# Optimization experiments

Measured on AMD Instinct MI355X. Metric: run time of the kernel, lower is better.

Reference implementation:

```python
import jax, jax.numpy as jnp
import numpy as np

D_MODEL = 1024
H = 16
D_K = D_MODEL // H

def setup_inputs() -> dict:
    key = jax.random.key(0)
    k1, k2, k3, k4, k5 = jax.random.split(key, 5)
    x = jax.random.normal(k1, (2, 2048, D_MODEL), dtype=jnp.float32)
    s = 1.0 / np.sqrt(D_MODEL)
    W_qkv = jax.random.uniform(k2, (D_MODEL, 3 * D_MODEL), jnp.float32, -s, s)
    b_qkv = jax.random.uniform(k3, (3 * D_MODEL,), jnp.float32, -s, s)
    W_o = jax.random.uniform(k4, (D_MODEL, D_MODEL), jnp.float32, -s, s)
    b_o = jax.random.uniform(k5, (D_MODEL,), jnp.float32, -s, s)
    return {"x": x, "W_qkv": W_qkv, "b_qkv": b_qkv, "W_o": W_o, "b_o": b_o}

def reference(x, W_qkv, b_qkv, W_o, b_o):
    B, L, _ = x.shape
    qkv = x @ W_qkv + b_qkv                      # [B, L, 3*d_model]
    q, k, v = jnp.split(qkv, 3, axis=-1)
    def split_heads(t):
        return t.reshape(B, L, H, D_K).transpose(0, 2, 1, 3)  # [B,H,L,D_k]
    q, k, v = split_heads(q), split_heads(k), split_heads(v)
    scores = jnp.einsum('bhqd,bhkd->bhqk', q, k) / np.sqrt(D_K).astype(jnp.float32)
    attn = jax.nn.softmax(scores, axis=-1)       # [B,H,L,L]
    ctx = jnp.einsum('bhqk,bhkd->bhqd', attn, v)
    ctx = ctx.transpose(0, 2, 1, 3).reshape(B, L, H * D_K)
    out = ctx @ W_o + b_o                        # dropout is identity at eval
    return (out, attn)
```

## Files before the change

kernel.cpp:

```cpp
#include <hip/hip_runtime.h>
#include <stdint.h>

typedef __attribute__((ext_vector_type(8))) short bf16x8;
typedef __attribute__((ext_vector_type(4))) float f32x4;
typedef __attribute__((ext_vector_type(4))) unsigned int u32x4;
typedef __attribute__((ext_vector_type(4))) unsigned short u16x4;

#define DEVINL static __device__ __forceinline__

DEVINL unsigned short f2bf(float f) {
  uint32_t u = __builtin_bit_cast(uint32_t, f);
  u = (u + 0x7FFFu + ((u >> 16) & 1u)) >> 16;
  return (unsigned short)u;
}

DEVINL float fexp2(float x) {
#if __has_builtin(__builtin_amdgcn_exp2f)
  return __builtin_amdgcn_exp2f(x);
#else
  return __expf(x * 0.69314718056f);
#endif
}

DEVINL bf16x8 pack8(f32x4 a, f32x4 b) {
  union { uint32_t u[4]; bf16x8 v; } r;
  asm("v_cvt_pk_bf16_f32 %0, %1, %2" : "=v"(r.u[0]) : "v"(a[0]), "v"(a[1]));
  asm("v_cvt_pk_bf16_f32 %0, %1, %2" : "=v"(r.u[1]) : "v"(a[2]), "v"(a[3]));
  asm("v_cvt_pk_bf16_f32 %0, %1, %2" : "=v"(r.u[2]) : "v"(b[0]), "v"(b[1]));
  asm("v_cvt_pk_bf16_f32 %0, %1, %2" : "=v"(r.u[3]) : "v"(b[2]), "v"(b[3]));
  return r.v;
}

DEVINL void async16(const unsigned short* lds, const unsigned short* g) {
  __builtin_amdgcn_global_load_lds(
      (const __attribute__((address_space(1))) unsigned int*)g,
      (__attribute__((address_space(3))) unsigned int*)lds, 16, 0, 0);
}

__global__ __launch_bounds__(256) void k_cast_x(const float* __restrict__ in,
                                                unsigned short* __restrict__ out, int n4) {
  int i = blockIdx.x * 256 + threadIdx.x;
  if (i >= n4) return;
  f32x4 v = *(const f32x4*)(in + (size_t)i * 4);
  u16x4 o;
  for (int j = 0; j < 4; ++j) o[j] = f2bf(v[j]);
  *(u16x4*)(out + (size_t)i * 4) = o;
}

__global__ __launch_bounds__(256) void k_transpose_w(const float* __restrict__ in,
                                                     unsigned short* __restrict__ out,
                                                     int K, int N) {
  __shared__ unsigned short tile[64][72];
  int k0 = blockIdx.x * 64, n0 = blockIdx.y * 64;
  int t = threadIdx.x;
  int r = t >> 2, c0 = (t & 3) * 16;
  for (int j = 0; j < 4; ++j) {
    int col = c0 + j * 4;
    f32x4 v = *(const f32x4*)(in + (size_t)(k0 + r) * N + n0 + col);
    u16x4 o;
    for (int q = 0; q < 4; ++q) o[q] = f2bf(v[q]);
    *(u16x4*)(&tile[r][col]) = o;
  }
  __syncthreads();
  for (int j = 0; j < 4; ++j) {
    int kcol = c0 + j * 4;
    u16x4 o;
    for (int q = 0; q < 4; ++q) o[q] = tile[kcol + q][r];
    *(u16x4*)(out + (size_t)(n0 + r) * K + k0 + kcol) = o;
  }
}

template <int MODE>
__global__ __launch_bounds__(256) void k_gemm(const unsigned short* __restrict__ A,
                                              const unsigned short* __restrict__ Bt,
                                              const float* __restrict__ bias,
                                              unsigned short* __restrict__ Qb,
                                              unsigned short* __restrict__ Kb,
                                              unsigned short* __restrict__ Vt,
                                              float* __restrict__ outF) {
  constexpr int KD = 1024;
  __shared__ unsigned short sh[17408];
  unsigned short* lA = sh;
  unsigned short* lB = sh + 8192;
  int tid = threadIdx.x;
  int lane = tid & 63, w = tid >> 6;
  int wr = w >> 1, wc = w & 1;
  int m0 = blockIdx.x * 128, n0 = blockIdx.y * 128;
  int lr = lane & 15, lg = lane >> 4;

  f32x4 acc[4][4] = {};

  int srow = w * 32 + (lane >> 3);
  int scol = (lane & 7) * 8;
  const unsigned short* gA = A + (size_t)(m0 + srow) * KD + scol;
  const unsigned short* gB = Bt + (size_t)(n0 + srow) * KD + scol;

  for (int kk = 0; kk < KD; kk += 64) {
    for (int s = 0; s < 4; ++s) {
      async16(&lA[(w * 32 + s * 8) * 64], gA + (size_t)s * 8 * KD + kk);
      async16(&lB[(w * 32 + s * 8) * 64], gB + (size_t)s * 8 * KD + kk);
    }
    __syncthreads();
    for (int kq = 0; kq < 2; ++kq) {
      bf16x8 af[4], bfr[4];
      for (int i = 0; i < 4; ++i)
        af[i] = *(const bf16x8*)(&lA[(wr * 64 + i * 16 + lr) * 64 + (kq * 4 + lg) * 8]);
      for (int r = 0; r < 4; ++r)
        bfr[r] = *(const bf16x8*)(&lB[(wc * 64 + r * 16 + lr) * 64 + (kq * 4 + lg) * 8]);
      for (int i = 0; i < 4; ++i)
        for (int r = 0; r < 4; ++r)
          acc[i][r] = __builtin_amdgcn_mfma_f32_16x16x32_bf16(af[i], bfr[r], acc[i][r], 0, 0, 0);
    }
    __syncthreads();
  }

  if (MODE == 0) {
    int which = n0 >> 10;
    int head0 = (n0 & 1023) >> 6;
    int b_idx = m0 >> 11;
    int l0 = m0 & 2047;
    if (which < 2) {
      for (int r = 0; r < 4; ++r) {
        int nl = wc * 64 + r * 16 + lr;
        float bv = bias[n0 + nl];
        for (int i = 0; i < 4; ++i) {
          int mlb = wr * 64 + i * 16 + lg * 4;
          for (int jj = 0; jj < 4; ++jj)
            sh[(mlb + jj) * 136 + nl] = f2bf(acc[i][r][jj] + bv);
        }
      }
      __syncthreads();
      unsigned short* dst = (which == 0) ? Qb : Kb;
      for (int it = 0; it < 4; ++it) {
        int row = it * 64 + (tid >> 2);
        int ml = row & 127, hd = row >> 7;
        int c = (tid & 3) * 16;
        bf16x8 v0 = *(const bf16x8*)&sh[ml * 136 + hd * 64 + c];
        bf16x8 v1 = *(const bf16x8*)&sh[ml * 136 + hd * 64 + c + 8];
        size_t bh = (size_t)(b_idx * 16 + head0 + hd);
        size_t off = (bh * 2048 + l0 + ml) * 64 + c;
        *(bf16x8*)(dst + off) = v0;
        *(bf16x8*)(dst + off + 8) = v1;
      }
    } else {
      for (int r = 0; r < 4; ++r) {
        int nl = wc * 64 + r * 16 + lr;
        float bv = bias[n0 + nl];
        for (int i = 0; i < 4; ++i) {
          int mlb = wr * 64 + i * 16 + lg * 4;
          u16x4 pk;
          for (int jj = 0; jj < 4; ++jj) pk[jj] = f2bf(acc[i][r][jj] + bv);
          *(u16x4*)&sh[nl * 136 + mlb] = pk;
        }
      }
      __syncthreads();
      for (int it = 0; it < 4; ++it) {
        int nl = it * 32 + (tid >> 3);
        int c = (tid & 7) * 16;
        bf16x8 v0 = *(const bf16x8*)&sh[nl * 136 + c];
        bf16x8 v1 = *(const bf16x8*)&sh[nl * 136 + c + 8];
        int dk = nl & 63, hd = nl >> 6;
        size_t bh = (size_t)(b_idx * 16 + head0 + hd);
        size_t off = (bh * 64 + dk) * 2048 + l0 + c;
        *(bf16x8*)(Vt + off) = v0;
        *(bf16x8*)(Vt + off + 8) = v1;
      }
    }
  } else {
    for (int r = 0; r < 4; ++r) {
      int n = n0 + wc * 64 + r * 16 + lr;
      float bv = bias[n];
      for (int i = 0; i < 4; ++i) {
        int mb = m0 + wr * 64 + i * 16 + lg * 4;
        for (int jj = 0; jj < 4; ++jj)
          outF[(size_t)(mb + jj) * 1024 + n] = acc[i][r][jj] + bv;
      }
    }
  }
}

__global__ __launch_bounds__(256) void k_attn(const unsigned short* __restrict__ Qb,
                                              const unsigned short* __restrict__ Kb,
                                              const unsigned short* __restrict__ Vt,
                                              float* __restrict__ attn,
                                              unsigned short* __restrict__ ctx) {
  __shared__ unsigned short Ks[64 * 64];
  __shared__ unsigned short Vs[64 * 64];
  __shared__ float Pf[4][32 * 68];
  int tid = threadIdx.x, lane = tid & 63, w = tid >> 6;
  int lr = lane & 15, lg = lane >> 4;
  int bid = blockIdx.x;
  int xcd = bid & 7, slot = bid >> 3;
  int bh = xcd * 4 + (slot >> 4);
  int qb = slot & 15;
  int q0 = qb * 128 + w * 32;
  int b_idx = bh >> 4, h = bh & 15;
  const unsigned short* Qh = Qb + (size_t)bh * 2048 * 64;
  const unsigned short* Kh = Kb + (size_t)bh * 2048 * 64;
  const unsigned short* Vh = Vt + (size_t)bh * 64 * 2048;
  float* Pw = &Pf[w][0];
  const float A2 = 0.125f * 1.44269504089f;
  int e7 = lr & 7;

  int srow = w * 8 + (lane >> 3);
  int sc = (lane & 7) ^ (srow & 7);
  const unsigned short* gK = Kh + (size_t)srow * 64 + sc * 8;
  const unsigned short* gV = Vh + (size_t)srow * 2048 + sc * 8;

  bf16x8 qf[2][2];
  for (int i = 0; i < 2; ++i)
    for (int kq = 0; kq < 2; ++kq)
      qf[i][kq] = *(const bf16x8*)(Qh + (size_t)(q0 + i * 16 + lr) * 64 + kq * 32 + lg * 8);

  float l_run[8] = {0.f, 0.f, 0.f, 0.f, 0.f, 0.f, 0.f, 0.f};

  for (int kt = 0; kt < 32; ++kt) {
    async16(&Ks[(w * 8) * 64],       gK + (size_t)kt * 4096);
    async16(&Ks[((w + 4) * 8) * 64], gK + (size_t)kt * 4096 + 2048);
    __syncthreads();
    f32x4 acc[2][4] = {};
    for (int kq = 0; kq < 2; ++kq) {
      int j = kq * 4 + lg;
      bf16x8 kf[4];
      for (int r = 0; r < 4; ++r)
        kf[r] = *(const bf16x8*)&Ks[(r * 16 + lr) * 64 + ((j ^ e7) << 3)];
      for (int i = 0; i < 2; ++i)
        for (int r = 0; r < 4; ++r)
          acc[i][r] = __builtin_amdgcn_mfma_f32_16x16x32_bf16(qf[i][kq], kf[r], acc[i][r], 0, 0, 0);
    }
    for (int i = 0; i < 2; ++i)
      for (int jj = 0; jj < 4; ++jj) {
        int z = i * 4 + jj;
        l_run[z] += fexp2(acc[i][0][jj] * A2) + fexp2(acc[i][1][jj] * A2) +
                    fexp2(acc[i][2][jj] * A2) + fexp2(acc[i][3][jj] * A2);
      }
    __syncthreads();
  }
  float invl[8];
  for (int z = 0; z < 8; ++z) {
    float s = l_run[z];
    s += __shfl_xor(s, 1);
    s += __shfl_xor(s, 2);
    s += __shfl_xor(s, 4);
    s += __shfl_xor(s, 8);
    invl[z] = 1.0f / s;
  }

  f32x4 cacc[2][4] = {};
  float* attn_base = attn + (size_t)bh * 2048 * 2048;
  float* arow = attn_base + (size_t)(q0 + lg) * 2048 + lr * 4;

  for (int kt = 0; kt < 32; ++kt) {
    async16(&Ks[(w * 8) * 64],       gK + (size_t)kt * 4096);
    async16(&Ks[((w + 4) * 8) * 64], gK + (size_t)kt * 4096 + 2048);
    async16(&Vs[(w * 8) * 64],       gV + (size_t)kt * 64);
    async16(&Vs[((w + 4) * 8) * 64], gV + (size_t)kt * 64 + 65536);
    __syncthreads();
    f32x4 acc[2][4] = {};
    for (int kq = 0; kq < 2; ++kq) {
      int j = kq * 4 + lg;
      bf16x8 kf[4];
      for (int r = 0; r < 4; ++r)
        kf[r] = *(const bf16x8*)&Ks[(r * 16 + lr) * 64 + ((j ^ e7) << 3)];
      for (int i = 0; i < 2; ++i)
        for (int r = 0; r < 4; ++r)
          acc[i][r] = __builtin_amdgcn_mfma_f32_16x16x32_bf16(qf[i][kq], kf[r], acc[i][r], 0, 0, 0);
    }
    for (int i = 0; i < 2; ++i)
      for (int r = 0; r < 4; ++r) {
        int key = r * 16 + lr;
        for (int jj = 0; jj < 4; ++jj) {
          int z = i * 4 + jj;
          int rl = i * 16 + lg * 4 + jj;
          Pw[rl * 68 + key] = fexp2(acc[i][r][jj] * A2) * invl[z];
        }
      }
    for (int s = 0; s < 8; ++s) {
      f32x4 v = *(const f32x4*)(&Pw[(s * 4 + lg) * 68 + lr * 4]);
      __builtin_nontemporal_store(v, (f32x4*)(arow + (size_t)s * 4 * 2048 + kt * 64));
    }
    for (int kq2 = 0; kq2 < 2; ++kq2) {
      int j = kq2 * 4 + lg;
      int kof = kq2 * 32 + lg * 8;
      bf16x8 pa[2], vf[4];
      for (int i = 0; i < 2; ++i) {
        f32x4 plo = *(const f32x4*)(&Pw[(i * 16 + lr) * 68 + kof]);
        f32x4 phi = *(const f32x4*)(&Pw[(i * 16 + lr) * 68 + kof + 4]);
        pa[i] = pack8(plo, phi);
      }
      for (int nn = 0; nn < 4; ++nn)
        vf[nn] = *(const bf16x8*)&Vs[(nn * 16 + lr) * 64 + ((j ^ e7) << 3)];
      for (int i = 0; i < 2; ++i)
        for (int nn = 0; nn < 4; ++nn)
          cacc[i][nn] = __builtin_amdgcn_mfma_f32_16x16x32_bf16(pa[i], vf[nn], cacc[i][nn], 0, 0, 0);
    }
    __syncthreads();
  }

  for (int nn = 0; nn < 4; ++nn) {
    int d = nn * 16 + lr;
    for (int i = 0; i < 2; ++i)
      for (int jj = 0; jj < 4; ++jj) {
        int q = q0 + i * 16 + lg * 4 + jj;
        int tok = b_idx * 2048 + q;
        ctx[(size_t)tok * 1024 + h * 64 + d] = f2bf(cacc[i][nn][jj]);
      }
  }
}

extern "C" void kernel_launch(void* const* d_in, const int* in_sizes, int n_in,
                              void* d_out, int out_size, void* d_ws, size_t ws_size,
                              hipStream_t stream) {
  const float* x    = (const float*)d_in[0];
  const float* Wqkv = (const float*)d_in[1];
  const float* bqkv = (const float*)d_in[2];
  const float* Wo   = (const float*)d_in[3];
  const float* bo   = (const float*)d_in[4];
  float* out  = (float*)d_out;
  float* attn = out + (size_t)4096 * 1024;

  char* ws = (char*)d_ws;
  unsigned short* xbf = (unsigned short*)(ws);
  unsigned short* wqT = (unsigned short*)(ws + 8388608);
  unsigned short* woT = (unsigned short*)(ws + 14680064);
  unsigned short* Qb  = (unsigned short*)(ws + 16777216);
  unsigned short* Kb  = (unsigned short*)(ws + 25165824);
  unsigned short* Vt  = (unsigned short*)(ws + 33554432);
  unsigned short* ctx = (unsigned short*)(ws + 41943040);

  k_cast_x<<<dim3(4096), dim3(256), 0, stream>>>(x, xbf, 1048576);
  k_transpose_w<<<dim3(16, 48), dim3(256), 0, stream>>>(Wqkv, wqT, 1024, 3072);
  k_transpose_w<<<dim3(16, 16), dim3(256), 0, stream>>>(Wo, woT, 1024, 1024);
  k_gemm<0><<<dim3(32, 24), dim3(256), 0, stream>>>(xbf, wqT, bqkv, Qb, Kb, Vt, nullptr);
  k_attn<<<dim3(512), dim3(256), 0, stream>>>(Qb, Kb, Vt, attn, ctx);
  k_gemm<1><<<dim3(32, 8), dim3(256), 0, stream>>>(ctx, woT, bo, nullptr, nullptr, nullptr, out);
}
```

Before: 243.1 us.

## Double-buffer K/V tiles in attention with explicit vmcnt waits

Converts both attention passes to double-buffered LDS tiles. The next K (and V) tile is prefetched asynchronously while the current one is consumed, with hand-counted s_waitcnt vmcnt values that account for the outstanding nontemporal attn stores. The trailing __syncthreads is replaced by an LDS-only wait plus a raw barrier, so the loop no longer drains global stores. This hides global-load latency, at the cost of twice the K/V LDS and fragile wait counts that depend on exact instruction ordering.

Measured after the change: 240.3 us. No clear change (-1.2%).

```diff
diff --git a/kernel.cpp b/kernel.cpp
--- a/kernel.cpp
+++ b/kernel.cpp
@@ -20,6 +20,17 @@
 #else
   return __expf(x * 0.69314718056f);
 #endif
+}
+
+DEVINL void raw_barrier() {
+  __builtin_amdgcn_sched_barrier(0);
+  __builtin_amdgcn_s_barrier();
+  __builtin_amdgcn_sched_barrier(0);
+}
+
+DEVINL void barrier_lds_only() {
+  asm volatile("s_waitcnt lgkmcnt(0)" ::: "memory");
+  raw_barrier();
 }
 
 DEVINL bf16x8 pack8(f32x4 a, f32x4 b) {
@@ -184,8 +195,8 @@
                                               const unsigned short* __restrict__ Vt,
                                               float* __restrict__ attn,
                                               unsigned short* __restrict__ ctx) {
-  __shared__ unsigned short Ks[64 * 64];
-  __shared__ unsigned short Vs[64 * 64];
+  __shared__ unsigned short Ks[2][4096];
+  __shared__ unsigned short Vs[2][4096];
   __shared__ float Pf[4][32 * 68];
   int tid = threadIdx.x, lane = tid & 63, w = tid >> 6;
   int lr = lane & 15, lg = lane >> 4;
@@ -214,16 +225,24 @@
 
   float l_run[8] = {0.f, 0.f, 0.f, 0.f, 0.f, 0.f, 0.f, 0.f};
 
+  async16(&Ks[0][(w * 8) * 64],       gK);
+  async16(&Ks[0][((w + 4) * 8) * 64], gK + 2048);
   for (int kt = 0; kt < 32; ++kt) {
-    async16(&Ks[(w * 8) * 64],       gK + (size_t)kt * 4096);
-    async16(&Ks[((w + 4) * 8) * 64], gK + (size_t)kt * 4096 + 2048);
-    __syncthreads();
+    int cur = kt & 1;
+    if (kt < 31) {
+      async16(&Ks[cur ^ 1][(w * 8) * 64],       gK + (size_t)(kt + 1) * 4096);
+      async16(&Ks[cur ^ 1][((w + 4) * 8) * 64], gK + (size_t)(kt + 1) * 4096 + 2048);
+      asm volatile("s_waitcnt vmcnt(2)" ::: "memory");
+    } else {
+      asm volatile("s_waitcnt vmcnt(0)" ::: "memory");
+    }
+    raw_barrier();
     f32x4 acc[2][4] = {};
     for (int kq = 0; kq < 2; ++kq) {
       int j = kq * 4 + lg;
       bf16x8 kf[4];
       for (int r = 0; r < 4; ++r)
-        kf[r] = *(const bf16x8*)&Ks[(r * 16 + lr) * 64 + ((j ^ e7) << 3)];
+        kf[r] = *(const bf16x8*)&Ks[cur][(r * 16 + lr) * 64 + ((j ^ e7) << 3)];
       for (int i = 0; i < 2; ++i)
         for (int r = 0; r < 4; ++r)
           acc[i][r] = __builtin_amdgcn_mfma_f32_16x16x32_bf16(qf[i][kq], kf[r], acc[i][r], 0, 0, 0);
@@ -234,7 +253,7 @@
         l_run[z] += fexp2(acc[i][0][jj] * A2) + fexp2(acc[i][1][jj] * A2) +
                     fexp2(acc[i][2][jj] * A2) + fexp2(acc[i][3][jj] * A2);
       }
-    __syncthreads();
+    barrier_lds_only();
   }
   float invl[8];
   for (int z = 0; z < 8; ++z) {
@@ -250,18 +269,28 @@
   float* attn_base = attn + (size_t)bh * 2048 * 2048;
   float* arow = attn_base + (size_t)(q0 + lg) * 2048 + lr * 4;
 
+  async16(&Ks[0][(w * 8) * 64],       gK);
+  async16(&Ks[0][((w + 4) * 8) * 64], gK + 2048);
+  async16(&Vs[0][(w * 8) * 64],       gV);
+  async16(&Vs[0][((w + 4) * 8) * 64], gV + 65536);
   for (int kt = 0; kt < 32; ++kt) {
-    async16(&Ks[(w * 8) * 64],       gK + (size_t)kt * 4096);
-    async16(&Ks[((w + 4) * 8) * 64], gK + (size_t)kt * 4096 + 2048);
-    async16(&Vs[(w * 8) * 64],       gV + (size_t)kt * 64);
-    async16(&Vs[((w + 4) * 8) * 64], gV + (size_t)kt * 64 + 65536);
-    __syncthreads();
+    int cur = kt & 1;
+    if (kt < 31) {
+      async16(&Ks[cur ^ 1][(w * 8) * 64],       gK + (size_t)(kt + 1) * 4096);
+      async16(&Ks[cur ^ 1][((w + 4) * 8) * 64], gK + (size_t)(kt + 1) * 4096 + 2048);
+      async16(&Vs[cur ^ 1][(w * 8) * 64],       gV + (size_t)(kt + 1) * 64);
+      async16(&Vs[cur ^ 1][((w + 4) * 8) * 64], gV + (size_t)(kt + 1) * 64 + 65536);
+    }
+    if (kt == 0)       asm volatile("s_waitcnt vmcnt(4)" ::: "memory");
+    else if (kt == 31) asm volatile("s_waitcnt vmcnt(8)" ::: "memory");
+    else               asm volatile("s_waitcnt vmcnt(12)" ::: "memory");
+    raw_barrier();
     f32x4 acc[2][4] = {};
     for (int kq = 0; kq < 2; ++kq) {
       int j = kq * 4 + lg;
       bf16x8 kf[4];
       for (int r = 0; r < 4; ++r)
-        kf[r] = *(const bf16x8*)&Ks[(r * 16 + lr) * 64 + ((j ^ e7) << 3)];
+        kf[r] = *(const bf16x8*)&Ks[cur][(r * 16 + lr) * 64 + ((j ^ e7) << 3)];
       for (int i = 0; i < 2; ++i)
         for (int r = 0; r < 4; ++r)
           acc[i][r] = __builtin_amdgcn_mfma_f32_16x16x32_bf16(qf[i][kq], kf[r], acc[i][r], 0, 0, 0);
@@ -289,12 +318,12 @@
         pa[i] = pack8(plo, phi);
       }
       for (int nn = 0; nn < 4; ++nn)
-        vf[nn] = *(const bf16x8*)&Vs[(nn * 16 + lr) * 64 + ((j ^ e7) << 3)];
+        vf[nn] = *(const bf16x8*)&Vs[cur][(nn * 16 + lr) * 64 + ((j ^ e7) << 3)];
       for (int i = 0; i < 2; ++i)
         for (int nn = 0; nn < 4; ++nn)
           cacc[i][nn] = __builtin_amdgcn_mfma_f32_16x16x32_bf16(pa[i], vf[nn], cacc[i][nn], 0, 0, 0);
     }
-    __syncthreads();
+    barrier_lds_only();
   }
 
   for (int nn = 0; nn < 4; ++nn) {
```
